# Optimization experiments

Measured on AMD Instinct MI355X. Metric: run time of the kernel, lower is better.

Reference implementation:

```python
import jax, jax.numpy as jnp
import numpy as np

N_NODES = 50000
N_EDGES = 200000
N_GRAPHS = 2048
EMB = 300
N_LAYERS = 5
BN_EPS = 1e-5


def setup_inputs() -> dict:
    key = jax.random.key(0)
    ks = jax.random.split(key, 16)
    s = 0.02
    d = {}
    d["atomic_number"] = jax.random.randint(ks[0], (N_NODES,), 0, 120)
    d["chirality_type"] = jax.random.randint(ks[1], (N_NODES,), 0, 3)
    d["bond_type"] = jax.random.randint(ks[2], (N_EDGES,), 0, 6)
    d["bond_direction_type"] = jax.random.randint(ks[3], (N_EDGES,), 0, 3)
    d["src"] = jax.random.randint(ks[4], (N_EDGES,), 0, N_NODES)
    d["dst"] = jax.random.randint(ks[5], (N_EDGES,), 0, N_NODES)
    d["graph_ids"] = jnp.sort(jax.random.randint(ks[6], (N_NODES,), 0, N_GRAPHS))
    d["num_graphs"] = N_GRAPHS
    d["node_emb0"] = jax.random.normal(ks[7], (120, EMB), jnp.float32) * s
    d["node_emb1"] = jax.random.normal(ks[8], (3, EMB), jnp.float32) * s
    d["edge_emb0"] = jax.random.normal(ks[9], (N_LAYERS, 6, EMB), jnp.float32) * s
    d["edge_emb1"] = jax.random.normal(ks[10], (N_LAYERS, 3, EMB), jnp.float32) * s
    d["W1"] = jax.random.normal(ks[11], (N_LAYERS, EMB, 2 * EMB), jnp.float32) * s
    d["b1"] = jnp.zeros((N_LAYERS, 2 * EMB), jnp.float32)
    d["W2"] = jax.random.normal(ks[12], (N_LAYERS, 2 * EMB, EMB), jnp.float32) * s
    d["b2"] = jnp.zeros((N_LAYERS, EMB), jnp.float32)
    d["bn_gamma"] = jnp.ones((N_LAYERS, EMB), jnp.float32)
    d["bn_beta"] = jnp.zeros((N_LAYERS, EMB), jnp.float32)
    d["bn_mean"] = jax.random.normal(ks[13], (N_LAYERS, EMB), jnp.float32) * s
    d["bn_var"] = jax.random.uniform(ks[14], (N_LAYERS, EMB), jnp.float32, 0.5, 1.5)
    return d


def gin_node_feats(atomic_number, chirality_type, bond_type, bond_direction_type,
                   src, dst, node_emb0, node_emb1, edge_emb0, edge_emb1,
                   W1, b1, W2, b2, bn_gamma, bn_beta, bn_mean, bn_var):
    n = atomic_number.shape[0]
    h = node_emb0[atomic_number] + node_emb1[chirality_type]  # [N, EMB]
    feats = [h]
    for l in range(N_LAYERS):
        # u_add_e message: src node feat + per-layer categorical edge embedding
        e = edge_emb0[l][bond_type] + edge_emb1[l][bond_direction_type]  # [E, EMB]
        m = feats[l][src] + e
        agg = jax.ops.segment_sum(m, dst, num_segments=n)  # sum aggregation at dst
        x = jax.nn.relu(agg @ W1[l] + b1[l]) @ W2[l] + b2[l]  # GIN MLP 300->600->300
        # BatchNorm1d in eval mode (running stats)
        x = (x - bn_mean[l]) * jax.lax.rsqrt(bn_var[l] + BN_EPS) * bn_gamma[l] + bn_beta[l]
        if l < N_LAYERS - 1:
            x = jax.nn.relu(x)  # activation on all but last layer
        feats.append(x)  # dropout is identity in eval mode
    return jnp.concatenate(feats, axis=1)  # JK='concat' -> [N, 6*EMB]


def reference(atomic_number, chirality_type, bond_type, bond_direction_type,
              src, dst, graph_ids, num_graphs,
              node_emb0, node_emb1, edge_emb0, edge_emb1,
              W1, b1, W2, b2, bn_gamma, bn_beta, bn_mean, bn_var):
    nf = gin_node_feats(atomic_number, chirality_type, bond_type, bond_direction_type,
                        src, dst, node_emb0, node_emb1, edge_emb0, edge_emb1,
                        W1, b1, W2, b2, bn_gamma, bn_beta, bn_mean, bn_var)
    sums = jax.ops.segment_sum(nf, graph_ids, num_segments=num_graphs)  # SumPooling
    counts = jax.ops.segment_sum(jnp.ones((nf.shape[0], 1), nf.dtype), graph_ids,
                                 num_segments=num_graphs)
    avg = sums / jnp.maximum(counts, 1.0)  # AvgPooling
    return jnp.concatenate([avg, sums], axis=1)  # [G, 2*6*EMB]
```

## Files before the change

### kernel.cpp

```cpp
#include <hip/hip_runtime.h>

#define EMB 300
#define HID 600
#define NL 5
#define BN_EPS 1e-5f

#define FS 320
#define HS 640
#define W2ROWS 384
#define NPW 8

typedef __attribute__((ext_vector_type(8))) short short8;
typedef __attribute__((ext_vector_type(4))) float f32x4;
typedef __attribute__((ext_vector_type(4))) unsigned short us4;

__device__ __forceinline__ unsigned short f2bf(float x) {
    unsigned u = __float_as_uint(x);
    unsigned r = (u + 0x7FFFu + ((u >> 16) & 1u)) >> 16;
    return (unsigned short)r;
}
__device__ __forceinline__ float bf2f(unsigned short h) {
    return __uint_as_float(((unsigned)h) << 16);
}

#define GLDS16(gsrc, ldst)                                                     \
    __builtin_amdgcn_global_load_lds(                                          \
        (const __attribute__((address_space(1))) unsigned int*)(gsrc),         \
        (__attribute__((address_space(3))) unsigned int*)(ldst), 16, 0, 0)

__global__ void k_init_h0(const int* __restrict__ an, const int* __restrict__ ch,
                          const float* __restrict__ ne0, const float* __restrict__ ne1,
                          unsigned short* __restrict__ Fb, int n) {
    int t = blockIdx.x * blockDim.x + threadIdx.x;
    int i = t / (FS / 4), f4 = t - i * (FS / 4);
    if (i >= n) return;
    int f = f4 * 4;
    us4 h = {0, 0, 0, 0};
    if (f < EMB) {
        const float4 a = *(const float4*)(ne0 + (size_t)an[i] * EMB + f);
        const float4 b = *(const float4*)(ne1 + (size_t)ch[i] * EMB + f);
        h[0] = f2bf(a.x + b.x); h[1] = f2bf(a.y + b.y);
        h[2] = f2bf(a.z + b.z); h[3] = f2bf(a.w + b.w);
    }
    *(us4*)(Fb + (size_t)i * FS + f) = h;
}

__global__ void k_hist(const int* __restrict__ dst, const int* __restrict__ bt,
                       const int* __restrict__ bd, int* __restrict__ deg,
                       int* __restrict__ cnt9, int e) {
    int t = blockIdx.x * blockDim.x + threadIdx.x;
    if (t >= e) return;
    int d = dst[t];
    atomicAdd(&deg[d], 1);
    atomicAdd(&cnt9[d * 9 + bt[t]], 1);
    atomicAdd(&cnt9[d * 9 + 6 + bd[t]], 1);
}

__global__ __launch_bounds__(256)
void k_scan_blk(const int* __restrict__ deg, int* __restrict__ incl,
                int* __restrict__ part, int n) {
    int tid = threadIdx.x;
    int base = blockIdx.x * 1024 + tid * 4;
    int v0 = (base + 0 < n) ? deg[base + 0] : 0;
    int v1 = (base + 1 < n) ? deg[base + 1] : 0;
    int v2 = (base + 2 < n) ? deg[base + 2] : 0;
    int v3 = (base + 3 < n) ? deg[base + 3] : 0;
    int ts = v0 + v1 + v2 + v3;
    int lane = tid & 63, w = tid >> 6;
    int x = ts;
#pragma unroll
    for (int off = 1; off < 64; off <<= 1) {
        int y = __shfl_up(x, off);
        if (lane >= off) x += y;
    }
    __shared__ int ws[4];
    if (lane == 63) ws[w] = x;
    __syncthreads();
    int woff = 0;
    for (int i = 0; i < w; ++i) woff += ws[i];
    int r = woff + x - ts;
    r += v0; if (base + 0 < n) incl[base + 0] = r;
    r += v1; if (base + 1 < n) incl[base + 1] = r;
    r += v2; if (base + 2 < n) incl[base + 2] = r;
    r += v3; if (base + 3 < n) incl[base + 3] = r;
    if (tid == 255) part[blockIdx.x] = woff + x;
}

__global__ __launch_bounds__(1024)
void k_scan_part(int* __restrict__ part, int nb) {
    int tid = threadIdx.x;
    int v = (tid < nb) ? part[tid] : 0;
    int lane = tid & 63, w = tid >> 6;
    int x = v;
#pragma unroll
    for (int off = 1; off < 64; off <<= 1) {
        int y = __shfl_up(x, off);
        if (lane >= off) x += y;
    }
    __shared__ int ws[16];
    if (lane == 63) ws[w] = x;
    __syncthreads();
    int woff = 0;
    for (int i = 0; i < w; ++i) woff += ws[i];
    if (tid < nb) part[tid] = woff + x - v;
}

__global__ void k_scan_add(const int* __restrict__ incl, const int* __restrict__ part,
                           const int* __restrict__ deg, int* __restrict__ roff,
                           int* __restrict__ curs, int n) {
    int i = blockIdx.x * blockDim.x + threadIdx.x;
    if (i >= n) return;
    int inc = incl[i] + part[i >> 10];
    roff[i + 1] = inc;
    curs[i] = inc - deg[i];
    if (i == 0) roff[0] = 0;
}

__global__ void k_scatter(const int* __restrict__ dst, const int* __restrict__ src,
                          int* __restrict__ cursor, int* __restrict__ srcs, int e) {
    int t = blockIdx.x * blockDim.x + threadIdx.x;
    if (t < e) { int p = atomicAdd(&cursor[dst[t]], 1); srcs[p] = src[t]; }
}

__global__ void k_gbound(const int* __restrict__ gids, int* __restrict__ gstart,
                         int n, int G) {
    int i = blockIdx.x * blockDim.x + threadIdx.x;
    if (i >= n) return;
    int g = gids[i];
    int gp = (i == 0) ? -1 : gids[i - 1];
    for (int q = gp + 1; q <= g; ++q) gstart[q] = i;
    if (i == n - 1)
        for (int q = g + 1; q <= G; ++q) gstart[q] = n;
}

__global__ void k_prep_w1(const float* __restrict__ W1, unsigned short* __restrict__ W1T, int total) {
    int t = blockIdx.x * blockDim.x + threadIdx.x;
    if (t >= total) return;
    int k = t % FS, n = (t / FS) % HS, l = t / (FS * HS);
    W1T[t] = (n < HID && k < EMB) ? f2bf(W1[l * (EMB * HID) + k * HID + n]) : 0;
}

__global__ void k_prep_w2(const float* __restrict__ W2, unsigned short* __restrict__ W2T, int total) {
    int t = blockIdx.x * blockDim.x + threadIdx.x;
    if (t >= total) return;
    int k = t % HS, n = (t / HS) % W2ROWS, l = t / (HS * W2ROWS);
    W2T[t] = (n < EMB && k < HID) ? f2bf(W2[l * (HID * EMB) + k * EMB + n]) : 0;
}

__global__ void k_prep_params(const float* __restrict__ b1, const float* __restrict__ b2,
                              const float* __restrict__ g, const float* __restrict__ be,
                              const float* __restrict__ mu, const float* __restrict__ va,
                              float* __restrict__ b1p, float* __restrict__ scp,
                              float* __restrict__ shp, int total) {
    int t = blockIdx.x * blockDim.x + threadIdx.x;
    if (t >= total) return;
    int n = t % HS, l = t / HS;
    b1p[t] = (n < HID) ? b1[l * HID + n] : 0.f;
    if (n < FS) {
        float sc = 0.f, sh = 0.f;
        if (n < EMB) {
            sc = g[l * EMB + n] * rsqrtf(va[l * EMB + n] + BN_EPS);
            sh = be[l * EMB + n] + (b2[l * EMB + n] - mu[l * EMB + n]) * sc;
        }
        scp[l * FS + n] = sc;
        shp[l * FS + n] = sh;
    }
}

__global__ __launch_bounds__(256)
void k_aggregate(const unsigned short* __restrict__ fb,
                 const float* __restrict__ e0,
                 const float* __restrict__ e1,
                 const int* __restrict__ roff, const int* __restrict__ srcs,
                 const int* __restrict__ cnt9,
                 unsigned short* __restrict__ agg,
                 int n) {
    const int v0 = (blockIdx.x * 4 + (threadIdx.x >> 6)) * NPW;
    if (v0 >= n) return;
    const int lane = threadIdx.x & 63;
    const int nv = min(NPW, n - v0);

    int rv = 0;
    {
        int idx = v0 + lane;
        if (lane <= NPW && idx <= n) rv = roff[idx];
    }
    const int base = __shfl(rv, 0);
    const int total = __shfl(rv, nv) - base;

    const int n9 = n * 9;
    const int base9 = v0 * 9;
    int c0 = (base9 + lane < n9) ? cnt9[base9 + lane] : 0;
    int c1 = (lane < 8 && base9 + 64 + lane < n9) ? cnt9[base9 + 64 + lane] : 0;

    int c = 0;
    int chunk = 0;
    auto nextIdx = [&]() -> int {
        if ((c & 63) == 0)
            chunk = (c + lane < total) ? srcs[base + c + lane] : 0;
        int r = __shfl(chunk, c & 63);
        ++c;
        return r;
    };

#pragma unroll
    for (int i = 0; i < NPW; ++i) {
        if (i < nv) {
            const int di = __shfl(rv, i + 1) - __shfl(rv, i);
            float aA[4] = {0.f, 0.f, 0.f, 0.f};
            float aB[4] = {0.f, 0.f, 0.f, 0.f};
            int k = 0;
            for (; k + 4 <= di; k += 4) {
                int i0 = nextIdx(), i1 = nextIdx(), i2 = nextIdx(), i3 = nextIdx();
                const us4* r0 = (const us4*)(fb + (size_t)i0 * FS);
                const us4* r1 = (const us4*)(fb + (size_t)i1 * FS);
                const us4* r2 = (const us4*)(fb + (size_t)i2 * FS);
                const us4* r3 = (const us4*)(fb + (size_t)i3 * FS);
                us4 x0 = r0[lane], x1 = r1[lane], x2 = r2[lane], x3 = r3[lane];
                us4 y0 = {}, y1 = {}, y2 = {}, y3 = {};
                if (lane < 11) { y0 = r0[64 + lane]; y1 = r1[64 + lane];
                                 y2 = r2[64 + lane]; y3 = r3[64 + lane]; }
#pragma unroll
                for (int q = 0; q < 4; ++q)
                    aA[q] += (bf2f(x0[q]) + bf2f(x1[q])) + (bf2f(x2[q]) + bf2f(x3[q]));
                if (lane < 11) {
#pragma unroll
                    for (int q = 0; q < 4; ++q)
                        aB[q] += (bf2f(y0[q]) + bf2f(y1[q])) + (bf2f(y2[q]) + bf2f(y3[q]));
                }
            }
            for (; k < di; ++k) {
                int i0 = nextIdx();
                const us4* r0 = (const us4*)(fb + (size_t)i0 * FS);
                us4 x0 = r0[lane];
#pragma unroll
                for (int q = 0; q < 4; ++q) aA[q] += bf2f(x0[q]);
                if (lane < 11) {
                    us4 y0 = r0[64 + lane];
#pragma unroll
                    for (int q = 0; q < 4; ++q) aB[q] += bf2f(y0[q]);
                }
            }
#pragma unroll
            for (int t = 0; t < 9; ++t) {
                const int pos = i * 9 + t;
                int cv = __shfl(pos < 64 ? c0 : c1, pos & 63);
                if (cv) {
                    float fc = (float)cv;
                    const float* row = (t < 6) ? (e0 + t * EMB) : (e1 + (t - 6) * EMB);
                    f32x4 ea = *(const f32x4*)(row + 4 * lane);
#pragma unroll
                    for (int q = 0; q < 4; ++q) aA[q] += fc * ea[q];
                    if (lane < 11) {
                        f32x4 eb = *(const f32x4*)(row + 256 + 4 * lane);
#pragma unroll
                        for (int q = 0; q < 4; ++q) aB[q] += fc * eb[q];
                    }
                }
            }
            us4* ar = (us4*)(agg + (size_t)(v0 + i) * FS);
            us4 h;
#pragma unroll
            for (int q = 0; q < 4; ++q) h[q] = f2bf(aA[q]);
            ar[lane] = h;
            if (lane < 11) {
                us4 hb;
#pragma unroll
                for (int q = 0; q < 4; ++q) hb[q] = f2bf(aB[q]);
                ar[64 + lane] = hb;
            }
        }
    }
}

template <int EPI>
__global__ __launch_bounds__(512)
void k_mm(const unsigned short* __restrict__ A, int lda,
          const unsigned short* __restrict__ Bt, int ldb,
          const float* __restrict__ p0, const float* __restrict__ p1,
          unsigned short* __restrict__ Cb, int ldc, int K, int Nlim,
          int MT, int NT) {
    const int d = blockIdx.x;
    const int xcd = d & 7, slot = d >> 3;
    const int pi = slot / NT, in = slot - pi * NT;
    const int im = pi * 8 + xcd;
    if (im >= MT) return;

    __shared__ unsigned short As[3][256 * 32];
    __shared__ unsigned short Bs[3][128 * 32];
    const int tid = threadIdx.x;
    const int lane = tid & 63, wid = tid >> 6;
    const int wm = wid >> 1, wn = wid & 1;
    const size_t bm = (size_t)im * 256;
    const int bn = in * 128;
    const int lr = lane & 15, lk = lane >> 4;
    const int srow = lane >> 2;
    const int scol = (lane & 3) * 8;
    f32x4 acc[4][4] = {};

    const unsigned short* gA  = A + (bm + (size_t)(wid * 16 + srow)) * lda + scol;
    const unsigned short* gA2 = A + (bm + (size_t)((wid + 8) * 16 + srow)) * lda + scol;
    const unsigned short* gB  = Bt + (size_t)(bn + wid * 16 + srow) * ldb + scol;

    auto STAGE = [&](int buf, int k0) {
        GLDS16(gA  + k0, &As[buf][(wid * 16) * 32]);
        GLDS16(gA2 + k0, &As[buf][((wid + 8) * 16) * 32]);
        GLDS16(gB  + k0, &Bs[buf][(wid * 16) * 32]);
    };

    const int nt = K >> 5;
    STAGE(0, 0);
    if (nt > 1) STAGE(1, 32);

    for (int t = 0; t < nt; ++t) {
        if (t + 1 < nt) asm volatile("s_waitcnt vmcnt(3)" ::: "memory");
        else            asm volatile("s_waitcnt vmcnt(0)" ::: "memory");
        __builtin_amdgcn_s_barrier();
        const int cur = t % 3;
        short8 a[4], b[4];
#pragma unroll
        for (int j = 0; j < 4; ++j)
            a[j] = *(const short8*)&As[cur][(wm * 64 + j * 16 + lr) * 32 + lk * 8];
#pragma unroll
        for (int i = 0; i < 4; ++i)
            b[i] = *(const short8*)&Bs[cur][(wn * 64 + i * 16 + lr) * 32 + lk * 8];
        if (t + 2 < nt) STAGE((t + 2) % 3, (t + 2) * 32);
        __builtin_amdgcn_s_setprio(1);
#pragma unroll
        for (int i = 0; i < 4; ++i)
#pragma unroll
            for (int j = 0; j < 4; ++j)
                acc[i][j] = __builtin_amdgcn_mfma_f32_16x16x32_bf16(b[i], a[j], acc[i][j], 0, 0, 0);
        __builtin_amdgcn_s_setprio(0);
    }

    const int rgrp = (lane >> 4) * 4;
#pragma unroll
    for (int i = 0; i < 4; ++i) {
        const int n0 = bn + wn * 64 + i * 16 + rgrp;
        if (EPI != 0 && n0 >= Nlim) continue;
        const f32x4 q0 = *(const f32x4*)&p0[n0];
        f32x4 q1 = {};
        if (EPI != 0) q1 = *(const f32x4*)&p1[n0];
#pragma unroll
        for (int j = 0; j < 4; ++j) {
            const size_t m = bm + (size_t)(wm * 64 + j * 16 + lr);
            us4 h;
#pragma unroll
            for (int p = 0; p < 4; ++p) {
                float x = (EPI == 0) ? (acc[i][j][p] + q0[p]) : (acc[i][j][p] * q0[p] + q1[p]);
                if (EPI != 2) x = fmaxf(x, 0.f);
                h[p] = f2bf(x);
            }
            *(us4*)(Cb + m * ldc + n0) = h;
        }
    }
}

__global__ __launch_bounds__(256)
void k_pool(const unsigned short* __restrict__ feats, const int* __restrict__ gstart,
            float* __restrict__ out, int l) {
    const int g = blockIdx.x;
    const int tid = threadIdx.x;
    const int w = tid >> 6, lane = tid & 63;
    const int s = gstart[g], e = gstart[g + 1];
    float aA[4] = {0.f, 0.f, 0.f, 0.f};
    float aB[4] = {0.f, 0.f, 0.f, 0.f};
    int v = s + w;
    for (; v + 4 < e; v += 8) {
        const us4* r0 = (const us4*)(feats + (size_t)v * FS);
        const us4* r1 = (const us4*)(feats + (size_t)(v + 4) * FS);
        us4 x0 = r0[lane], x1 = r1[lane];
        us4 y0 = {}, y1 = {};
        if (lane < 11) { y0 = r0[64 + lane]; y1 = r1[64 + lane]; }
#pragma unroll
        for (int q = 0; q < 4; ++q) aA[q] += bf2f(x0[q]) + bf2f(x1[q]);
        if (lane < 11) {
#pragma unroll
            for (int q = 0; q < 4; ++q) aB[q] += bf2f(y0[q]) + bf2f(y1[q]);
        }
    }
    if (v < e) {
        const us4* r0 = (const us4*)(feats + (size_t)v * FS);
        us4 x0 = r0[lane];
#pragma unroll
        for (int q = 0; q < 4; ++q) aA[q] += bf2f(x0[q]);
        if (lane < 11) {
            us4 y0 = r0[64 + lane];
#pragma unroll
            for (int q = 0; q < 4; ++q) aB[q] += bf2f(y0[q]);
        }
    }
    __shared__ f32x4 smA[4][64];
    __shared__ f32x4 smB[4][16];
    f32x4 xa;
#pragma unroll
    for (int q = 0; q < 4; ++q) xa[q] = aA[q];
    smA[w][lane] = xa;
    if (lane < 16) {
        f32x4 xb;
#pragma unroll
        for (int q = 0; q < 4; ++q) xb[q] = aB[q];
        smB[w][lane] = xb;
    }
    __syncthreads();
    if (w == 0) {
        f32x4 t = smA[0][lane] + smA[1][lane] + smA[2][lane] + smA[3][lane];
        float inv = 1.0f / fmaxf((float)(e - s), 1.0f);
        float* oavg = out + (size_t)g * (12 * EMB) + l * EMB;
        float* osum = oavg + 6 * EMB;
        *(f32x4*)(oavg + 4 * lane) = t * inv;
        *(f32x4*)(osum + 4 * lane) = t;
        if (lane < 11) {
            f32x4 tb = smB[0][lane] + smB[1][lane] + smB[2][lane] + smB[3][lane];
            *(f32x4*)(oavg + 256 + 4 * lane) = tb * inv;
            *(f32x4*)(osum + 256 + 4 * lane) = tb;
        }
    }
}

extern "C" void kernel_launch(void* const* d_in, const int* in_sizes, int n_in,
                              void* d_out, int out_size, void* d_ws, size_t ws_size,
                              hipStream_t stream) {
    const int*   an  = (const int*)d_in[0];
    const int*   ch  = (const int*)d_in[1];
    const int*   bt  = (const int*)d_in[2];
    const int*   bd  = (const int*)d_in[3];
    const int*   src = (const int*)d_in[4];
    const int*   dst = (const int*)d_in[5];
    const int*   gid = (const int*)d_in[6];
    const float* ne0 = (const float*)d_in[8];
    const float* ne1 = (const float*)d_in[9];
    const float* ee0 = (const float*)d_in[10];
    const float* ee1 = (const float*)d_in[11];
    const float* W1  = (const float*)d_in[12];
    const float* b1  = (const float*)d_in[13];
    const float* W2  = (const float*)d_in[14];
    const float* b2  = (const float*)d_in[15];
    const float* bng = (const float*)d_in[16];
    const float* bnb = (const float*)d_in[17];
    const float* bnm = (const float*)d_in[18];
    const float* bnv = (const float*)d_in[19];

    const int N = in_sizes[0];
    const int E = in_sizes[2];
    const int G = out_size / (12 * EMB);
    const int M_pad = ((N + 255) / 256) * 256;
    const int MT = M_pad / 256;
    const int MT8 = ((MT + 7) / 8) * 8;
    const int nb = (N + 1023) / 1024;

    char* ws = (char*)d_ws;
    size_t off = 0;
    auto alloc = [&](size_t bytes) -> void* {
        void* p = (void*)(ws + off);
        off += (bytes + 255) & ~(size_t)255;
        return p;
    };
    unsigned short* Fb0  = (unsigned short*)alloc((size_t)M_pad * FS * 2);
    unsigned short* Fb1  = (unsigned short*)alloc((size_t)M_pad * FS * 2);
    unsigned short* A1   = (unsigned short*)alloc((size_t)M_pad * FS * 2);
    unsigned short* Hb   = (unsigned short*)alloc((size_t)M_pad * HS * 2);
    unsigned short* W1T  = (unsigned short*)alloc((size_t)NL * HS * FS * 2);
    unsigned short* W2T  = (unsigned short*)alloc((size_t)NL * W2ROWS * HS * 2);
    float*          b1p  = (float*)alloc((size_t)NL * HS * 4);
    float*          scp  = (float*)alloc((size_t)NL * FS * 4);
    float*          shp  = (float*)alloc((size_t)NL * FS * 4);
    int*            deg  = (int*)alloc((size_t)N * 4);
    int*            roff = (int*)alloc(((size_t)N + 1) * 4);
    int*            curs = (int*)alloc((size_t)N * 4);
    int*            srcs = (int*)alloc((size_t)E * 4);
    int*            cnt9 = (int*)alloc((size_t)N * 9 * 4);
    int*            incl = (int*)alloc((size_t)N * 4);
    int*            part = (int*)alloc((size_t)1024 * 4);
    int*            gst  = (int*)alloc(((size_t)G + 1) * 4);

    {
        int t1 = NL * HS * FS;
        k_prep_w1<<<(t1 + 255) / 256, 256, 0, stream>>>(W1, W1T, t1);
        int t2 = NL * W2ROWS * HS;
        k_prep_w2<<<(t2 + 255) / 256, 256, 0, stream>>>(W2, W2T, t2);
        int t3 = NL * HS;
        k_prep_params<<<(t3 + 255) / 256, 256, 0, stream>>>(b1, b2, bng, bnb, bnm, bnv,
                                                            b1p, scp, shp, t3);
    }

    {
        int tt = N * (FS / 4);
        k_init_h0<<<(tt + 255) / 256, 256, 0, stream>>>(an, ch, ne0, ne1, Fb0, N);
    }

    hipMemsetAsync(deg, 0, (size_t)N * 4, stream);
    hipMemsetAsync(cnt9, 0, (size_t)N * 9 * 4, stream);
    k_hist<<<(E + 255) / 256, 256, 0, stream>>>(dst, bt, bd, deg, cnt9, E);
    k_scan_blk<<<nb, 256, 0, stream>>>(deg, incl, part, N);
    k_scan_part<<<1, 1024, 0, stream>>>(part, nb);
    k_scan_add<<<(N + 255) / 256, 256, 0, stream>>>(incl, part, deg, roff, curs, N);
    k_scatter<<<(E + 255) / 256, 256, 0, stream>>>(dst, src, curs, srcs, E);
    k_gbound<<<(N + 255) / 256, 256, 0, stream>>>(gid, gst, N, G);

    const int NT1 = HS / 128;
    const int NT2 = W2ROWS / 128;
    const int aggBlocks = (N + 4 * NPW - 1) / (4 * NPW);

    unsigned short* Fbc = Fb0;
    unsigned short* Fbo = Fb1;
    for (int l = 0; l < NL; ++l) {
        k_pool<<<G, 256, 0, stream>>>(Fbc, gst, (float*)d_out, l);
        k_aggregate<<<aggBlocks, 256, 0, stream>>>(Fbc,
                                                   ee0 + (size_t)l * 6 * EMB,
                                                   ee1 + (size_t)l * 3 * EMB,
                                                   roff, srcs, cnt9, A1, N);
        k_mm<0><<<MT8 * NT1, 512, 0, stream>>>(A1, FS, W1T + (size_t)l * HS * FS, FS,
                                               b1p + (size_t)l * HS, nullptr, Hb, HS,
                                               FS, HS, MT, NT1);
        if (l < NL - 1)
            k_mm<1><<<MT8 * NT2, 512, 0, stream>>>(Hb, HS, W2T + (size_t)l * W2ROWS * HS, HS,
                                                   scp + (size_t)l * FS, shp + (size_t)l * FS,
                                                   Fbo, FS, HS, FS, MT, NT2);
        else
            k_mm<2><<<MT8 * NT2, 512, 0, stream>>>(Hb, HS, W2T + (size_t)l * W2ROWS * HS, HS,
                                                   scp + (size_t)l * FS, shp + (size_t)l * FS,
                                                   Fbo, FS, HS, FS, MT, NT2);
        unsigned short* t = Fbc; Fbc = Fbo; Fbo = t;
    }
    k_pool<<<G, 256, 0, stream>>>(Fbc, gst, (float*)d_out, NL);
}
```

Measured before the change: 760.8 us.

## Fuse two-layer MLP GEMMs into one kernel keeping hidden activations in LDS

```diff
diff --git a/kernel.cpp b/kernel.cpp
--- a/kernel.cpp
+++ b/kernel.cpp
@@ -7,8 +7,9 @@
 
 #define FS 320
 #define HS 640
-#define W2ROWS 384
 #define NPW 8
+#define KS1 10
+#define KS2 20
 
 typedef __attribute__((ext_vector_type(8))) short short8;
 typedef __attribute__((ext_vector_type(4))) float f32x4;
@@ -133,18 +134,44 @@
         for (int q = g + 1; q <= G; ++q) gstart[q] = n;
 }
 
-__global__ void k_prep_w1(const float* __restrict__ W1, unsigned short* __restrict__ W1T, int total) {
+__global__ void k_prep_w1p(const float* __restrict__ W1, unsigned short* __restrict__ W1P,
+                           int total) {
     int t = blockIdx.x * blockDim.x + threadIdx.x;
     if (t >= total) return;
-    int k = t % FS, n = (t / FS) % HS, l = t / (FS * HS);
-    W1T[t] = (n < HID && k < EMB) ? f2bf(W1[l * (EMB * HID) + k * HID + n]) : 0;
-}
-
-__global__ void k_prep_w2(const float* __restrict__ W2, unsigned short* __restrict__ W2T, int total) {
+    int lane = t & 63;
+    int r = t >> 6;
+    int ks = r % KS1; r /= KS1;
+    int nf = r % 40;
+    int l = r / 40;
+    int n = nf * 16 + (lane & 15);
+    int kb = ks * 32 + (lane >> 4) * 8;
+    unsigned short v[8];
+#pragma unroll
+    for (int e = 0; e < 8; ++e) {
+        int k = kb + e;
+        v[e] = (n < HID && k < EMB) ? f2bf(W1[(size_t)l * EMB * HID + (size_t)k * HID + n]) : 0;
+    }
+    *(short8*)(W1P + (size_t)t * 8) = *(short8*)v;
+}
+
+__global__ void k_prep_w2p(const float* __restrict__ W2, unsigned short* __restrict__ W2P,
+                           int total) {
     int t = blockIdx.x * blockDim.x + threadIdx.x;
     if (t >= total) return;
-    int k = t % HS, n = (t / HS) % W2ROWS, l = t / (HS * W2ROWS);
-    W2T[t] = (n < EMB && k < HID) ? f2bf(W2[l * (HID * EMB) + k * EMB + n]) : 0;
+    int lane = t & 63;
+    int r = t >> 6;
+    int ks = r % KS2; r /= KS2;
+    int nf = r % 20;
+    int l = r / 20;
+    int n = nf * 16 + (lane & 15);
+    int kb = ks * 32 + (lane >> 4) * 8;
+    unsigned short v[8];
+#pragma unroll
+    for (int e = 0; e < 8; ++e) {
+        int k = kb + e;
+        v[e] = (n < EMB && k < HID) ? f2bf(W2[(size_t)l * HID * EMB + (size_t)k * EMB + n]) : 0;
+    }
+    *(short8*)(W2P + (size_t)t * 8) = *(short8*)v;
 }
 
 __global__ void k_prep_params(const float* __restrict__ b1, const float* __restrict__ b2,
@@ -169,12 +196,10 @@
 
 __global__ __launch_bounds__(256)
 void k_aggregate(const unsigned short* __restrict__ fb,
-                 const float* __restrict__ e0,
-                 const float* __restrict__ e1,
+                 const float* __restrict__ e0, const float* __restrict__ e1,
                  const int* __restrict__ roff, const int* __restrict__ srcs,
                  const int* __restrict__ cnt9,
-                 unsigned short* __restrict__ agg,
-                 int n) {
+                 unsigned short* __restrict__ agg, int n) {
     const int v0 = (blockIdx.x * 4 + (threadIdx.x >> 6)) * NPW;
     if (v0 >= n) return;
     const int lane = threadIdx.x & 63;
@@ -275,84 +300,120 @@
 
 template <int EPI>
 __global__ __launch_bounds__(512)
-void k_mm(const unsigned short* __restrict__ A, int lda,
-          const unsigned short* __restrict__ Bt, int ldb,
-          const float* __restrict__ p0, const float* __restrict__ p1,
-          unsigned short* __restrict__ Cb, int ldc, int K, int Nlim,
-          int MT, int NT) {
-    const int d = blockIdx.x;
-    const int xcd = d & 7, slot = d >> 3;
-    const int pi = slot / NT, in = slot - pi * NT;
-    const int im = pi * 8 + xcd;
-    if (im >= MT) return;
-
-    __shared__ unsigned short As[3][256 * 32];
-    __shared__ unsigned short Bs[3][128 * 32];
+void k_mlp(const unsigned short* __restrict__ A,
+           const unsigned short* __restrict__ W1P,
+           const unsigned short* __restrict__ W2P,
+           const float* __restrict__ b1p,
+           const float* __restrict__ scp, const float* __restrict__ shp,
+           unsigned short* __restrict__ Cout) {
+    __shared__ unsigned short Ash[64 * 320];
+    __shared__ unsigned short Hsh[64 * 640];
     const int tid = threadIdx.x;
     const int lane = tid & 63, wid = tid >> 6;
-    const int wm = wid >> 1, wn = wid & 1;
-    const size_t bm = (size_t)im * 256;
-    const int bn = in * 128;
-    const int lr = lane & 15, lk = lane >> 4;
-    const int srow = lane >> 2;
-    const int scol = (lane & 3) * 8;
-    f32x4 acc[4][4] = {};
-
-    const unsigned short* gA  = A + (bm + (size_t)(wid * 16 + srow)) * lda + scol;
-    const unsigned short* gA2 = A + (bm + (size_t)((wid + 8) * 16 + srow)) * lda + scol;
-    const unsigned short* gB  = Bt + (size_t)(bn + wid * 16 + srow) * ldb + scol;
-
-    auto STAGE = [&](int buf, int k0) {
-        GLDS16(gA  + k0, &As[buf][(wid * 16) * 32]);
-        GLDS16(gA2 + k0, &As[buf][((wid + 8) * 16) * 32]);
-        GLDS16(gB  + k0, &Bs[buf][(wid * 16) * 32]);
-    };
-
-    const int nt = K >> 5;
-    STAGE(0, 0);
-    if (nt > 1) STAGE(1, 32);
-
-    for (int t = 0; t < nt; ++t) {
-        if (t + 1 < nt) asm volatile("s_waitcnt vmcnt(3)" ::: "memory");
-        else            asm volatile("s_waitcnt vmcnt(0)" ::: "memory");
-        __builtin_amdgcn_s_barrier();
-        const int cur = t % 3;
-        short8 a[4], b[4];
-#pragma unroll
-        for (int j = 0; j < 4; ++j)
-            a[j] = *(const short8*)&As[cur][(wm * 64 + j * 16 + lr) * 32 + lk * 8];
-#pragma unroll
-        for (int i = 0; i < 4; ++i)
-            b[i] = *(const short8*)&Bs[cur][(wn * 64 + i * 16 + lr) * 32 + lk * 8];
-        if (t + 2 < nt) STAGE((t + 2) % 3, (t + 2) * 32);
-        __builtin_amdgcn_s_setprio(1);
-#pragma unroll
-        for (int i = 0; i < 4; ++i)
-#pragma unroll
-            for (int j = 0; j < 4; ++j)
-                acc[i][j] = __builtin_amdgcn_mfma_f32_16x16x32_bf16(b[i], a[j], acc[i][j], 0, 0, 0);
-        __builtin_amdgcn_s_setprio(0);
-    }
-
-    const int rgrp = (lane >> 4) * 4;
-#pragma unroll
-    for (int i = 0; i < 4; ++i) {
-        const int n0 = bn + wn * 64 + i * 16 + rgrp;
-        if (EPI != 0 && n0 >= Nlim) continue;
-        const f32x4 q0 = *(const f32x4*)&p0[n0];
-        f32x4 q1 = {};
-        if (EPI != 0) q1 = *(const f32x4*)&p1[n0];
-#pragma unroll
-        for (int j = 0; j < 4; ++j) {
-            const size_t m = bm + (size_t)(wm * 64 + j * 16 + lr);
-            us4 h;
-#pragma unroll
-            for (int p = 0; p < 4; ++p) {
-                float x = (EPI == 0) ? (acc[i][j][p] + q0[p]) : (acc[i][j][p] * q0[p] + q1[p]);
-                if (EPI != 2) x = fmaxf(x, 0.f);
-                h[p] = f2bf(x);
-            }
-            *(us4*)(Cb + m * ldc + n0) = h;
+    const int lr = lane & 15, lk = lane >> 4, rgrp = lk * 4;
+    const size_t m0s = (size_t)blockIdx.x * 64;
+
+#pragma unroll
+    for (int cch = 0; cch < 5; ++cch) {
+        const int sbase = wid * 5120 + cch * 1024;
+        const int s = sbase + lane * 16;
+        const int row = s / 640;
+        const int u = s ^ ((row & 7) << 4);
+        GLDS16((const char*)A + m0s * 640 + u, (char*)Ash + sbase);
+    }
+    asm volatile("s_waitcnt vmcnt(0)" ::: "memory");
+    __syncthreads();
+
+    {
+        f32x4 acc1[5][4] = {};
+        short8 bw[5], bn_[5];
+#pragma unroll
+        for (int i = 0; i < 5; ++i)
+            bw[i] = *(const short8*)(W1P + (((size_t)(wid * 5 + i) * KS1 + 0) * 64 + lane) * 8);
+        for (int ks = 0; ks < KS1; ++ks) {
+            if (ks + 1 < KS1) {
+#pragma unroll
+                for (int i = 0; i < 5; ++i)
+                    bn_[i] = *(const short8*)(W1P + (((size_t)(wid * 5 + i) * KS1 + ks + 1) * 64 + lane) * 8);
+            }
+            short8 a[4];
+#pragma unroll
+            for (int j = 0; j < 4; ++j) {
+                const int row = j * 16 + lr;
+                const int o = (row * 640 + ks * 64 + lk * 16) ^ ((lr & 7) << 4);
+                a[j] = *(const short8*)((const char*)Ash + o);
+            }
+#pragma unroll
+            for (int i = 0; i < 5; ++i)
+#pragma unroll
+                for (int j = 0; j < 4; ++j)
+                    acc1[i][j] = __builtin_amdgcn_mfma_f32_16x16x32_bf16(bw[i], a[j], acc1[i][j], 0, 0, 0);
+#pragma unroll
+            for (int i = 0; i < 5; ++i) bw[i] = bn_[i];
+        }
+#pragma unroll
+        for (int i = 0; i < 5; ++i) {
+            const int n0 = wid * 80 + i * 16 + rgrp;
+            const f32x4 q0 = *(const f32x4*)&b1p[n0];
+#pragma unroll
+            for (int j = 0; j < 4; ++j) {
+                const int m = j * 16 + lr;
+                us4 h;
+#pragma unroll
+                for (int p = 0; p < 4; ++p)
+                    h[p] = f2bf(fmaxf(acc1[i][j][p] + q0[p], 0.f));
+                const int o = (m * 1280 + n0 * 2) ^ ((lr & 7) << 4);
+                *(us4*)((char*)Hsh + o) = h;
+            }
+        }
+    }
+    __syncthreads();
+
+    {
+        const int wm2 = wid >> 2, wn2 = wid & 3;
+        f32x4 acc2[5][2] = {};
+        short8 cw[5], cn_[5];
+#pragma unroll
+        for (int i = 0; i < 5; ++i)
+            cw[i] = *(const short8*)(W2P + (((size_t)(wn2 * 5 + i) * KS2 + 0) * 64 + lane) * 8);
+        for (int ks = 0; ks < KS2; ++ks) {
+            if (ks + 1 < KS2) {
+#pragma unroll
+                for (int i = 0; i < 5; ++i)
+                    cn_[i] = *(const short8*)(W2P + (((size_t)(wn2 * 5 + i) * KS2 + ks + 1) * 64 + lane) * 8);
+            }
+            short8 a[2];
+#pragma unroll
+            for (int j = 0; j < 2; ++j) {
+                const int row = wm2 * 32 + j * 16 + lr;
+                const int o = (row * 1280 + ks * 64 + lk * 16) ^ ((lr & 7) << 4);
+                a[j] = *(const short8*)((const char*)Hsh + o);
+            }
+#pragma unroll
+            for (int i = 0; i < 5; ++i)
+#pragma unroll
+                for (int j = 0; j < 2; ++j)
+                    acc2[i][j] = __builtin_amdgcn_mfma_f32_16x16x32_bf16(cw[i], a[j], acc2[i][j], 0, 0, 0);
+#pragma unroll
+            for (int i = 0; i < 5; ++i) cw[i] = cn_[i];
+        }
+#pragma unroll
+        for (int i = 0; i < 5; ++i) {
+            const int n0 = wn2 * 80 + i * 16 + rgrp;
+            const f32x4 q0 = *(const f32x4*)&scp[n0];
+            const f32x4 q1 = *(const f32x4*)&shp[n0];
+#pragma unroll
+            for (int j = 0; j < 2; ++j) {
+                const size_t m = m0s + (size_t)(wm2 * 32 + j * 16 + lr);
+                us4 h;
+#pragma unroll
+                for (int p = 0; p < 4; ++p) {
+                    float x = acc2[i][j][p] * q0[p] + q1[p];
+                    if (EPI == 1) x = fmaxf(x, 0.f);
+                    h[p] = f2bf(x);
+                }
+                *(us4*)(Cout + m * FS + n0) = h;
+            }
         }
     }
 }
@@ -445,9 +506,8 @@
     const int N = in_sizes[0];
     const int E = in_sizes[2];
     const int G = out_size / (12 * EMB);
-    const int M_pad = ((N + 255) / 256) * 256;
-    const int MT = M_pad / 256;
-    const int MT8 = ((MT + 7) / 8) * 8;
+    const int M_pad = ((N + 63) / 64) * 64;
+    const int MT = M_pad / 64;
     const int nb = (N + 1023) / 1024;
 
     char* ws = (char*)d_ws;
@@ -460,9 +520,8 @@
     unsigned short* Fb0  = (unsigned short*)alloc((size_t)M_pad * FS * 2);
     unsigned short* Fb1  = (unsigned short*)alloc((size_t)M_pad * FS * 2);
     unsigned short* A1   = (unsigned short*)alloc((size_t)M_pad * FS * 2);
-    unsigned short* Hb   = (unsigned short*)alloc((size_t)M_pad * HS * 2);
-    unsigned short* W1T  = (unsigned short*)alloc((size_t)NL * HS * FS * 2);
-    unsigned short* W2T  = (unsigned short*)alloc((size_t)NL * W2ROWS * HS * 2);
+    unsigned short* W1P  = (unsigned short*)alloc((size_t)NL * 40 * KS1 * 64 * 8 * 2);
+    unsigned short* W2P  = (unsigned short*)alloc((size_t)NL * 20 * KS2 * 64 * 8 * 2);
     float*          b1p  = (float*)alloc((size_t)NL * HS * 4);
     float*          scp  = (float*)alloc((size_t)NL * FS * 4);
     float*          shp  = (float*)alloc((size_t)NL * FS * 4);
@@ -476,10 +535,10 @@
     int*            gst  = (int*)alloc(((size_t)G + 1) * 4);
 
     {
-        int t1 = NL * HS * FS;
-        k_prep_w1<<<(t1 + 255) / 256, 256, 0, stream>>>(W1, W1T, t1);
-        int t2 = NL * W2ROWS * HS;
-        k_prep_w2<<<(t2 + 255) / 256, 256, 0, stream>>>(W2, W2T, t2);
+        int t1 = NL * 40 * KS1 * 64;
+        k_prep_w1p<<<(t1 + 255) / 256, 256, 0, stream>>>(W1, W1P, t1);
+        int t2 = NL * 20 * KS2 * 64;
+        k_prep_w2p<<<(t2 + 255) / 256, 256, 0, stream>>>(W2, W2P, t2);
         int t3 = NL * HS;
         k_prep_params<<<(t3 + 255) / 256, 256, 0, stream>>>(b1, b2, bng, bnb, bnm, bnv,
                                                             b1p, scp, shp, t3);
@@ -499,8 +558,6 @@
     k_scatter<<<(E + 255) / 256, 256, 0, stream>>>(dst, src, curs, srcs, E);
     k_gbound<<<(N + 255) / 256, 256, 0, stream>>>(gid, gst, N, G);
 
-    const int NT1 = HS / 128;
-    const int NT2 = W2ROWS / 128;
     const int aggBlocks = (N + 4 * NPW - 1) / (4 * NPW);
 
     unsigned short* Fbc = Fb0;
@@ -511,17 +568,18 @@
                                                    ee0 + (size_t)l * 6 * EMB,
                                                    ee1 + (size_t)l * 3 * EMB,
                                                    roff, srcs, cnt9, A1, N);
-        k_mm<0><<<MT8 * NT1, 512, 0, stream>>>(A1, FS, W1T + (size_t)l * HS * FS, FS,
-                                               b1p + (size_t)l * HS, nullptr, Hb, HS,
-                                               FS, HS, MT, NT1);
+        const unsigned short* W1Pl = W1P + (size_t)l * 40 * KS1 * 64 * 8;
+        const unsigned short* W2Pl = W2P + (size_t)l * 20 * KS2 * 64 * 8;
         if (l < NL - 1)
-            k_mm<1><<<MT8 * NT2, 512, 0, stream>>>(Hb, HS, W2T + (size_t)l * W2ROWS * HS, HS,
-                                                   scp + (size_t)l * FS, shp + (size_t)l * FS,
-                                                   Fbo, FS, HS, FS, MT, NT2);
+            k_mlp<1><<<MT, 512, 0, stream>>>(A1, W1Pl, W2Pl,
+                                             b1p + (size_t)l * HS,
+                                             scp + (size_t)l * FS, shp + (size_t)l * FS,
+                                             Fbo);
         else
-            k_mm<2><<<MT8 * NT2, 512, 0, stream>>>(Hb, HS, W2T + (size_t)l * W2ROWS * HS, HS,
-                                                   scp + (size_t)l * FS, shp + (size_t)l * FS,
-                                                   Fbo, FS, HS, FS, MT, NT2);
+            k_mlp<2><<<MT, 512, 0, stream>>>(A1, W1Pl, W2Pl,
+                                             b1p + (size_t)l * HS,
+                                             scp + (size_t)l * FS, shp + (size_t)l * FS,
+                                             Fbo);
         unsigned short* t = Fbc; Fbc = Fbo; Fbo = t;
     }
     k_pool<<<G, 256, 0, stream>>>(Fbc, gst, (float*)d_out, NL);
```

Measured after the change: 755.3 us. About the same (-0.7%).
